# Kernel tuning notes

Measured on AMD Instinct MI355X. Metric: run time of the kernel, lower is better.

Reference implementation:

```python
import jax, jax.numpy as jnp
import numpy as np

B, T, E, H, D, NL = 2, 1024, 2048, 16, 128, 3
MAXL = T * (2 ** (NL - 1))  # k length doubles each layer: T, 2T, 4T


def _rms_norm(x, w, eps=1e-5):
    return x * jax.lax.rsqrt(jnp.mean(x * x, axis=-1, keepdims=True) + eps) * w


def _rope(x, cos, sin):
    # x: [B, S, H, D]; cos/sin: [>=S, D/2]; GPT-NeoX style (non-interleaved)
    S = x.shape[1]
    c = cos[:S][None, :, None, :]
    s = sin[:S][None, :, None, :]
    x1, x2 = jnp.split(x, 2, axis=-1)
    return jnp.concatenate([x1 * c - x2 * s, x1 * s + x2 * c], axis=-1)


def _causal_attn(q, k, v):
    # bottom-right-aligned causal (flash_attn_func causal=True with kv longer than q)
    Tq, L = q.shape[1], k.shape[1]
    scale = 1.0 / np.sqrt(q.shape[-1]).astype(np.float32)
    scores = jnp.einsum('bthd,bshd->bhts', q, k) * scale
    i = jnp.arange(Tq)[:, None]
    j = jnp.arange(L)[None, :]
    mask = j <= i + (L - Tq)
    scores = jnp.where(mask[None, None], scores, -jnp.inf)
    p = jax.nn.softmax(scores, axis=-1)
    return jnp.einsum('bhts,bshd->bthd', p, v)


def setup_inputs() -> dict:
    key = jax.random.key(0)
    ks = jax.random.split(key, 6)
    x = jax.random.normal(ks[0], (B, T, E), dtype=jnp.float32)
    inv_freq = 1.0 / (10000.0 ** (np.arange(0, D, 2, dtype=np.float32) / D))  # [D/2]
    ang = np.arange(MAXL, dtype=np.float32)[:, None] * inv_freq[None, :]      # [MAXL, D/2]
    cos = jnp.asarray(np.cos(ang), dtype=jnp.float32)
    sin = jnp.asarray(np.sin(ang), dtype=jnp.float32)
    wq = jax.random.normal(ks[1], (NL, E, E), dtype=jnp.float32) * 0.02
    wk = jax.random.normal(ks[2], (NL, E, E), dtype=jnp.float32) * 0.02
    wv = jax.random.normal(ks[3], (NL, E, E), dtype=jnp.float32) * 0.02
    ln_w = jnp.ones((NL, E), dtype=jnp.float32)
    lambdas = jnp.zeros((NL,), dtype=jnp.float32)
    w_out = jax.random.normal(ks[4], (E, E), dtype=jnp.float32) * 0.02
    final_ln_w = jnp.ones((E,), dtype=jnp.float32)
    alpha = jnp.ones((1,), dtype=jnp.float32)
    return {'x': x, 'cos': cos, 'sin': sin, 'wq': wq, 'wk': wk, 'wv': wv,
            'ln_w': ln_w, 'lambdas': lambdas, 'w_out': w_out,
            'final_ln_w': final_ln_w, 'alpha': alpha}


def reference(x, cos, sin, wq, wk, wv, ln_w, lambdas, w_out, final_ln_w, alpha):
    bsz, tgt_len, embed_dim = x.shape
    # lambda weights: sigmoid then LayerNorm over the NL scalars (no affine)
    lam = jax.nn.sigmoid(lambdas)
    lam = (lam - jnp.mean(lam)) * jax.lax.rsqrt(jnp.var(lam) + 1e-5)
    acc_k, acc_v = [], []
    total = jnp.zeros_like(x)
    for i in range(NL):  # small fixed layer count
        q = (x @ wq[i].T).reshape(bsz, tgt_len, H, D)
        k = (x @ wk[i].T).reshape(bsz, tgt_len, H, D)
        v = (x @ wv[i].T).reshape(bsz, tgt_len, H, D)
        if i > 0:
            k = jnp.concatenate([k] + acc_k, axis=1)
            v = jnp.concatenate([v] + acc_v, axis=1)
        q = _rope(q, cos, sin)
        k = _rope(k, cos, sin)  # note: cached K gets rotary re-applied, as in source
        attn = _causal_attn(q, k, v).reshape(bsz, tgt_len, embed_dim)
        attn = _rms_norm(attn, ln_w[i])
        total = total + attn * lam[i]
        acc_k.append(k)
        acc_v.append(v)
    out = _rms_norm(total + alpha * x, final_ln_w)
    return out @ w_out.T
```

## Files before the change

kernel.cpp:

```cpp
#include <hip/hip_runtime.h>

typedef unsigned short ushort_t;
typedef __attribute__((ext_vector_type(8))) short bf16x8;
typedef __attribute__((ext_vector_type(4))) short bf16x4;
typedef __attribute__((ext_vector_type(4))) float f32x4;
typedef __attribute__((ext_vector_type(4))) unsigned short u16x4;
typedef __attribute__((ext_vector_type(4))) unsigned int u32x4;

#define DEV __device__ __forceinline__

DEV ushort_t f2bf(float f) {
  union { float f; unsigned int u; } a; a.f = f;
  unsigned int u = a.u;
  unsigned int r = (u + 0x7fffu + ((u >> 16) & 1u)) >> 16;
  return (ushort_t)r;
}
DEV float bf2f(ushort_t b) {
  union { float f; unsigned int u; } a; a.u = ((unsigned int)b) << 16;
  return a.f;
}
DEV void gload_lds16(const void* g, void* l) {
  __builtin_amdgcn_global_load_lds((const __attribute__((address_space(1))) void*)g,
                                   (__attribute__((address_space(3))) void*)l, 16, 0, 0);
}
DEV bf16x4 tr16(const ushort_t* l) {
  unsigned a = (unsigned)(unsigned long long)(const __attribute__((address_space(3))) ushort_t*)l;
  bf16x4 d;
  asm volatile("ds_read_b64_tr_b16 %0, %1" : "=v"(d) : "v"(a));
  return d;
}
DEV bf16x8 ldsb128(const ushort_t* l) {
  unsigned a = (unsigned)(unsigned long long)(const __attribute__((address_space(3))) ushort_t*)l;
  bf16x8 d;
  asm volatile("ds_read_b128 %0, %1" : "=v"(d) : "v"(a));
  return d;
}

__global__ __launch_bounds__(256) void f2b_kernel(const float* __restrict__ in,
                                                  ushort_t* __restrict__ out, int n) {
  int base = (blockIdx.x * 256 + threadIdx.x) * 4;
  if (base >= n) return;
  f32x4 v = *(const f32x4*)(in + base);
  u16x4 o;
  o.x = f2bf(v.x); o.y = f2bf(v.y); o.z = f2bf(v.z); o.w = f2bf(v.w);
  *(u16x4*)(out + base) = o;
}

__global__ __launch_bounds__(256) void f2b3_kernel(const float* __restrict__ a, const float* __restrict__ b,
                                                   const float* __restrict__ c, ushort_t* __restrict__ out) {
  int id = blockIdx.x * 256 + threadIdx.x;
  int sel = id >> 20, k = (id & 1048575) * 4;
  const float* src = sel == 0 ? a : sel == 1 ? b : c;
  f32x4 v = *(const f32x4*)(src + k);
  u16x4 o;
  o.x = f2bf(v.x); o.y = f2bf(v.y); o.z = f2bf(v.z); o.w = f2bf(v.w);
  *(u16x4*)(out + (size_t)sel * 4194304 + k) = o;
}

__global__ void lam_kernel(const float* __restrict__ lambdas, float* __restrict__ lam) {
  if (threadIdx.x == 0 && blockIdx.x == 0) {
    float l0 = 1.f / (1.f + __expf(-lambdas[0]));
    float l1 = 1.f / (1.f + __expf(-lambdas[1]));
    float l2 = 1.f / (1.f + __expf(-lambdas[2]));
    float mean = (l0 + l1 + l2) * (1.f / 3.f);
    float d0 = l0 - mean, d1 = l1 - mean, d2 = l2 - mean;
    float var = (d0 * d0 + d1 * d1 + d2 * d2) * (1.f / 3.f);
    float rs = rsqrtf(var + 1e-5f);
    lam[0] = d0 * rs; lam[1] = d1 * rs; lam[2] = d2 * rs;
  }
}

DEV void gemm_core(const ushort_t* __restrict__ A, const ushort_t* __restrict__ Bm,
                   ushort_t* lsA, ushort_t* lsB, int bm, int bn, int kbeg, int kend,
                   f32x4 (&acc)[4][4]) {
  const int K = 2048;
  int tid = threadIdx.x;
  int w = tid >> 6, lane = tid & 63;
  int g = lane >> 4, r = lane & 15;
  int wm = w >> 1, wn = w & 1;
#pragma unroll
  for (int i = 0; i < 4; ++i)
#pragma unroll
    for (int j = 0; j < 4; ++j) acc[i][j] = 0.f;

  for (int kk = kbeg; kk < kend; kk += 32) {
    __syncthreads();
#pragma unroll
    for (int j2 = 0; j2 < 2; ++j2) {
      int eb = w * 1024 + j2 * 512;
      int ebl = eb + lane * 8;
      int rr = ebl >> 5, cc = ebl & 31;
      gload_lds16(A + (size_t)(bm * 128 + rr) * K + kk + cc, lsA + eb);
      gload_lds16(Bm + (size_t)(bn * 128 + rr) * K + kk + cc, lsB + eb);
    }
    __syncthreads();
    bf16x8 af[4], bfr[4];
#pragma unroll
    for (int i = 0; i < 4; ++i)
      af[i] = *(const bf16x8*)(lsA + (wm * 64 + i * 16 + r) * 32 + g * 8);
#pragma unroll
    for (int j = 0; j < 4; ++j)
      bfr[j] = *(const bf16x8*)(lsB + (wn * 64 + j * 16 + r) * 32 + g * 8);
#pragma unroll
    for (int i = 0; i < 4; ++i)
#pragma unroll
      for (int j = 0; j < 4; ++j)
        acc[i][j] = __builtin_amdgcn_mfma_f32_16x16x32_bf16(af[i], bfr[j], acc[i][j], 0, 0, 0);
  }
}

__global__ __launch_bounds__(256) void gemm_qkv(
    const ushort_t* __restrict__ A,
    const ushort_t* __restrict__ Bq, const ushort_t* __restrict__ Bk, const ushort_t* __restrict__ Bv,
    ushort_t* __restrict__ Cq, ushort_t* __restrict__ Ck, ushort_t* __restrict__ Cv, int Lkv) {
  __shared__ __align__(16) ushort_t lsA[4096];
  __shared__ __align__(16) ushort_t lsB[4096];
  int sel = blockIdx.x >> 4, bn = blockIdx.x & 15, bm = blockIdx.y;
  const ushort_t* Bm = (sel == 0) ? Bq : (sel == 1) ? Bk : Bv;
  ushort_t* C = (sel == 0) ? Cq : (sel == 1) ? Ck : Cv;
  int Lsel = (sel == 0) ? 1024 : Lkv;
  f32x4 acc[4][4];
  gemm_core(A, Bm, lsA, lsB, bm, bn, 0, 2048, acc);
  int lane = threadIdx.x & 63, w = threadIdx.x >> 6;
  int g = lane >> 4, r = lane & 15, wm = w >> 1, wn = w & 1;
#pragma unroll
  for (int i = 0; i < 4; ++i)
#pragma unroll
    for (int j = 0; j < 4; ++j) {
      int row0 = bm * 128 + wm * 64 + i * 16 + g * 4;
      int col = bn * 128 + wn * 64 + j * 16 + r;
#pragma unroll
      for (int t = 0; t < 4; ++t) {
        int row = row0 + t;
        int b2 = row >> 10, t2 = row & 1023;
        C[(size_t)(b2 * Lsel + t2) * 2048 + col] = f2bf(acc[i][j][t]);
      }
    }
}

__global__ __launch_bounds__(256) void gemm_bt_part(
    const ushort_t* __restrict__ A, const ushort_t* __restrict__ Bm, float* __restrict__ P) {
  __shared__ __align__(16) ushort_t lsA[4096];
  __shared__ __align__(16) ushort_t lsB[4096];
  int bn = blockIdx.x, bm = blockIdx.y, s = blockIdx.z;
  f32x4 acc[4][4];
  gemm_core(A, Bm, lsA, lsB, bm, bn, s * 1024, (s + 1) * 1024, acc);
  float* C = P + (size_t)s * 4194304;
  int lane = threadIdx.x & 63, w = threadIdx.x >> 6;
  int g = lane >> 4, r = lane & 15, wm = w >> 1, wn = w & 1;
#pragma unroll
  for (int i = 0; i < 4; ++i)
#pragma unroll
    for (int j = 0; j < 4; ++j) {
      int row0 = bm * 128 + wm * 64 + i * 16 + g * 4;
      int col = bn * 128 + wn * 64 + j * 16 + r;
#pragma unroll
      for (int t = 0; t < 4; ++t)
        C[(size_t)(row0 + t) * 2048 + col] = acc[i][j][t];
    }
}

__global__ __launch_bounds__(256) void add2_kernel(const float* __restrict__ a, const float* __restrict__ b,
                                                   float* __restrict__ out) {
  int i = (blockIdx.x * 256 + threadIdx.x) * 4;
  f32x4 va = *(const f32x4*)(a + i);
  f32x4 vb = *(const f32x4*)(b + i);
  f32x4 r;
#pragma unroll
  for (int k = 0; k < 4; ++k) r[k] = va[k] + vb[k];
  *(f32x4*)(out + i) = r;
}

DEV void rope_body(const ushort_t* src, ushort_t* dst, const float* cosT, const float* sinT,
                   int Ls, int s0, int Ld, int dpos0, int cnt, int bp) {
  int b = bp / cnt, pidx = bp % cnt;
  int pos = dpos0 + pidx;
  int pi = threadIdx.x * 4;
  int h = pi >> 6, d = pi & 63;
  const ushort_t* s_ = src + ((size_t)(b * Ls + s0 + pidx) * 16 + h) * 128 + d;
  ushort_t* d_ = dst + ((size_t)(b * Ld + pos) * 16 + h) * 128 + d;
  f32x4 c4 = *(const f32x4*)(cosT + (size_t)pos * 64 + d);
  f32x4 s4 = *(const f32x4*)(sinT + (size_t)pos * 64 + d);
  u16x4 x1 = *(const u16x4*)(s_);
  u16x4 x2 = *(const u16x4*)(s_ + 64);
  u16x4 o1, o2;
#pragma unroll
  for (int k = 0; k < 4; ++k) {
    float a = bf2f(x1[k]), bb = bf2f(x2[k]);
    o1[k] = f2bf(a * c4[k] - bb * s4[k]);
    o2[k] = f2bf(a * s4[k] + bb * c4[k]);
  }
  *(u16x4*)d_ = o1;
  *(u16x4*)(d_ + 64) = o2;
}
DEV void copy_body(const ushort_t* src, ushort_t* dst, int Ls, int s0, int Ld, int dpos0,
                   int cnt, int bp) {
  int b = bp / cnt, pidx = bp % cnt;
  const u32x4* s = (const u32x4*)(src + (size_t)(b * Ls + s0 + pidx) * 2048);
  u32x4* d = (u32x4*)(dst + (size_t)(b * Ld + dpos0 + pidx) * 2048);
  d[threadIdx.x] = s[threadIdx.x];
}

__global__ __launch_bounds__(256) void rope_qk(ushort_t* q, ushort_t* Kc,
                                               const float* __restrict__ cosT, const float* __restrict__ sinT,
                                               int L) {
  int bp = blockIdx.x;
  if (bp < 2048) rope_body(q, q, cosT, sinT, 1024, 0, 1024, 0, 1024, bp);
  else rope_body(Kc, Kc, cosT, sinT, L, 0, L, 0, 1024, bp - 2048);
}

__global__ __launch_bounds__(256) void layer1_cache(const ushort_t* __restrict__ K0, ushort_t* __restrict__ K1,
                                                    const ushort_t* __restrict__ V0, ushort_t* __restrict__ V1,
                                                    const float* __restrict__ cosT, const float* __restrict__ sinT) {
  int bp = blockIdx.x;
  if (bp < 2048) rope_body(K0, K1, cosT, sinT, 1024, 0, 2048, 1024, 1024, bp);
  else copy_body(V0, V1, 1024, 0, 2048, 1024, 1024, bp - 2048);
}

__global__ __launch_bounds__(256) void layer2_cache(const ushort_t* __restrict__ K1, ushort_t* __restrict__ K2,
                                                    const ushort_t* __restrict__ V1, ushort_t* __restrict__ V2,
                                                    const float* __restrict__ cosT, const float* __restrict__ sinT) {
  int bp = blockIdx.x;
  if (bp < 2048) copy_body(K1, K2, 2048, 1024, 4096, 1024, 1024, bp);
  else if (bp < 6144) rope_body(K1, K2, cosT, sinT, 2048, 0, 4096, 2048, 2048, bp - 2048);
  else if (bp < 8192) copy_body(V1, V2, 2048, 1024, 4096, 1024, 1024, bp - 6144);
  else copy_body(V1, V2, 2048, 0, 4096, 2048, 2048, bp - 8192);
}

__global__ __launch_bounds__(256, 4) void attn_kernel(
    const ushort_t* __restrict__ Q, const ushort_t* __restrict__ Kc, const ushort_t* __restrict__ Vc,
    ushort_t* __restrict__ Opart, float2* __restrict__ Ml, int Lk) {
  __shared__ __align__(16) ushort_t lsK[8192];
  __shared__ __align__(16) ushort_t lsV[8192];
  const float sc = 0.08838834764831843f;

  int bid = (int)blockIdx.x;
  int swz = (bid & 7) * 128 + (bid >> 3);
  int s = swz & 1;
  int rest = swz >> 1;

  int w = threadIdx.x >> 6, lane = threadIdx.x & 63;
  int bq = rest & 15, h = (rest >> 4) & 15, b = rest >> 8;
  int qt = bq * 4 + w;
  int g = lane >> 4, r = lane & 15;
  int off = Lk - 1024;

  const ushort_t* qbase = Q + ((size_t)(b * 1024 + qt * 16 + r) * 16 + h) * 128;
  bf16x8 qf[4];
#pragma unroll
  for (int c = 0; c < 4; ++c) qf[c] = *(const bf16x8*)(qbase + c * 32 + g * 8);

  int t = threadIdx.x;
  int krow0 = t >> 4,        kc0 = (t & 15) ^ (krow0 & 7);
  int krow1 = (t + 256) >> 4, kc1 = (t & 15) ^ (krow1 & 7);
  const size_t adv = 32 * 2048;
  const size_t adv2 = 2 * adv;
  const ushort_t* srcK0 = Kc + ((size_t)(b * Lk + krow0) * 16 + h) * 128 + kc0 * 8 + s * adv;
  const ushort_t* srcK1 = Kc + ((size_t)(b * Lk + krow1) * 16 + h) * 128 + kc1 * 8 + s * adv;
  int L0 = t, L1 = t + 256;
  int vrow0 = ((L0 >> 3) & 7) * 4 + ((L0 >> 1) & 3), vd0 = (L0 >> 6) * 16 + (L0 & 1) * 8;
  int vrow1 = ((L1 >> 3) & 7) * 4 + ((L1 >> 1) & 3), vd1 = (L1 >> 6) * 16 + (L1 & 1) * 8;
  const ushort_t* srcV0 = Vc + ((size_t)(b * Lk + vrow0) * 16 + h) * 128 + vd0 + s * adv;
  const ushort_t* srcV1 = Vc + ((size_t)(b * Lk + vrow1) * 16 + h) * 128 + vd1 + s * adv;

  auto STAGE = [&](int buf) {
    ushort_t* k0 = lsK + buf * 4096 + w * 512;
    ushort_t* v0 = lsV + buf * 4096 + w * 512;
    gload_lds16(srcK0, k0);
    gload_lds16(srcK1, k0 + 2048);
    gload_lds16(srcV0, v0);
    gload_lds16(srcV1, v0 + 2048);
    srcK0 += adv2; srcK1 += adv2; srcV0 += adv2; srcV1 += adv2;
  };

  float m_run = -1e30f, l_run = 0.f;
  f32x4 o[8];
#pragma unroll
  for (int c = 0; c < 8; ++c) o[c] = 0.f;

  int qp = qt * 16 + r + off;
  int nkt_w = ((qt * 16 + 15 + off) >> 5) + 1;
  int nkt_blk = (((bq * 4 + 3) * 16 + 15 + off) >> 5) + 1;
  int ntile = (nkt_blk - s + 1) >> 1;

  if (ntile > 0) {
    STAGE(0);
    for (int it = 0; it < ntile; ++it) {
      int kt = s + it * 2;
      int cur = it & 1;
      if (it + 1 < ntile) {
        STAGE(cur ^ 1);
        asm volatile("s_waitcnt vmcnt(4)" ::: "memory");
      } else {
        asm volatile("s_waitcnt vmcnt(0)" ::: "memory");
      }
      __builtin_amdgcn_s_barrier();
      __builtin_amdgcn_sched_barrier(0);
      if (kt < nkt_w) {
        const ushort_t* Kb = lsK + cur * 4096;
        const ushort_t* Vb = lsV + cur * 4096;
        f32x4 st[2];
#pragma unroll
        for (int ks = 0; ks < 2; ++ks) {
          bf16x8 kf[4];
#pragma unroll
          for (int c = 0; c < 4; ++c)
            kf[c] = ldsb128(Kb + (ks * 16 + r) * 128 + ((c * 32 + g * 8) ^ ((r & 7) * 8)));
          asm volatile("s_waitcnt lgkmcnt(0)" ::: "memory");
          __builtin_amdgcn_sched_barrier(0);
          __builtin_amdgcn_s_setprio(1);
          f32x4 acc = 0.f;
#pragma unroll
          for (int c = 0; c < 4; ++c)
            acc = __builtin_amdgcn_mfma_f32_16x16x32_bf16(kf[c], qf[c], acc, 0, 0, 0);
          __builtin_amdgcn_s_setprio(0);
          st[ks] = acc;
        }
        float pmax = -1e30f;
        int kp0 = kt * 32;
#pragma unroll
        for (int ks = 0; ks < 2; ++ks)
#pragma unroll
          for (int j = 0; j < 4; ++j) {
            int key = kp0 + ks * 16 + g * 4 + j;
            float sv = st[ks][j] * sc;
            if (key > qp) sv = -1e30f;
            st[ks][j] = sv;
            pmax = fmaxf(pmax, sv);
          }
        pmax = fmaxf(pmax, __shfl_xor(pmax, 16, 64));
        pmax = fmaxf(pmax, __shfl_xor(pmax, 32, 64));
        if (!__all(pmax <= m_run + 8.f)) {
          float mnew = fmaxf(m_run, pmax);
          float corr = __expf(m_run - mnew);
          l_run *= corr;
#pragma unroll
          for (int c = 0; c < 8; ++c)
#pragma unroll
            for (int tt = 0; tt < 4; ++tt) o[c][tt] *= corr;
          m_run = mnew;
        }
        float psum = 0.f;
        bf16x4 pf[2];
#pragma unroll
        for (int ks = 0; ks < 2; ++ks)
#pragma unroll
          for (int j = 0; j < 4; ++j) {
            float pe = __expf(st[ks][j] - m_run);
            psum += pe;
            pf[ks][j] = (short)f2bf(pe);
          }
        psum += __shfl_xor(psum, 16, 64);
        psum += __shfl_xor(psum, 32, 64);
        l_run += psum;
#pragma unroll
        for (int half = 0; half < 2; ++half) {
          bf16x4 vf[8];
#pragma unroll
          for (int i = 0; i < 8; ++i)
            vf[i] = tr16(Vb + (half * 4 + (i >> 1)) * 512 + (i & 1) * 256);
          asm volatile("s_waitcnt lgkmcnt(0)" ::: "memory");
          __builtin_amdgcn_sched_barrier(0);
          __builtin_amdgcn_s_setprio(1);
#pragma unroll
          for (int db = 0; db < 4; ++db) {
            int dblk = half * 4 + db;
            o[dblk] = __builtin_amdgcn_mfma_f32_16x16x16bf16_1k(vf[db * 2], pf[0], o[dblk], 0, 0, 0);
            o[dblk] = __builtin_amdgcn_mfma_f32_16x16x16bf16_1k(vf[db * 2 + 1], pf[1], o[dblk], 0, 0, 0);
          }
          __builtin_amdgcn_s_setprio(0);
        }
      }
      __builtin_amdgcn_sched_barrier(0);
      __builtin_amdgcn_s_barrier();
    }
  }
  ushort_t* ob = Opart + (size_t)s * 4194304 + ((size_t)(b * 1024 + qt * 16 + r) * 16 + h) * 128;
#pragma unroll
  for (int dblk = 0; dblk < 8; ++dblk) {
    u16x4 ov;
#pragma unroll
    for (int tt = 0; tt < 4; ++tt) ov[tt] = f2bf(o[dblk][tt]);
    *(u16x4*)(ob + dblk * 16 + g * 4) = ov;
  }
  if (g == 0) {
    float2 ml; ml.x = m_run; ml.y = l_run;
    Ml[((size_t)(s * 2 + b) * 1024 + qt * 16 + r) * 16 + h] = ml;
  }
}

template <int FIRST>
__global__ __launch_bounds__(256) void rms_combine(const ushort_t* __restrict__ Opart, const float2* __restrict__ Ml,
                                                   const float* __restrict__ lnw, const float* __restrict__ lam,
                                                   int li, float* __restrict__ total) {
  int row = blockIdx.x;
  int t8 = threadIdx.x * 8;
  int h = t8 >> 7;
  float2 ml0 = Ml[(size_t)row * 16 + h];
  float2 ml1 = Ml[(size_t)(row + 2048) * 16 + h];
  float M = fmaxf(ml0.x, ml1.x);
  float w0 = __expf(ml0.x - M), w1 = __expf(ml1.x - M);
  float rinv = 1.f / (w0 * ml0.y + w1 * ml1.y);
  w0 *= rinv; w1 *= rinv;
  const ushort_t* a0 = Opart + (size_t)row * 2048 + t8;
  const ushort_t* a1 = a0 + 4194304;
  u16x4 p00 = *(const u16x4*)(a0);
  u16x4 p01 = *(const u16x4*)(a0 + 4);
  u16x4 p10 = *(const u16x4*)(a1);
  u16x4 p11 = *(const u16x4*)(a1 + 4);
  f32x4 v0, v1;
#pragma unroll
  for (int k = 0; k < 4; ++k) {
    v0[k] = w0 * bf2f(p00[k]) + w1 * bf2f(p10[k]);
    v1[k] = w0 * bf2f(p01[k]) + w1 * bf2f(p11[k]);
  }
  float ss = v0.x * v0.x + v0.y * v0.y + v0.z * v0.z + v0.w * v0.w +
             v1.x * v1.x + v1.y * v1.y + v1.z * v1.z + v1.w * v1.w;
#pragma unroll
  for (int m = 1; m < 64; m <<= 1) ss += __shfl_xor(ss, m, 64);
  __shared__ float red[4];
  int w = threadIdx.x >> 6, lane = threadIdx.x & 63;
  if (lane == 0) red[w] = ss;
  __syncthreads();
  ss = red[0] + red[1] + red[2] + red[3];
  float sca = rsqrtf(ss * (1.f / 2048.f) + 1e-5f) * lam[li];
  f32x4 w0v = *(const f32x4*)(lnw + t8);
  f32x4 w1v = *(const f32x4*)(lnw + t8 + 4);
  float* o = total + (size_t)row * 2048 + t8;
  f32x4 r0, r1;
#pragma unroll
  for (int k = 0; k < 4; ++k) { r0[k] = v0[k] * sca * w0v[k]; r1[k] = v1[k] * sca * w1v[k]; }
  if (!FIRST) {
    f32x4 q0 = *(const f32x4*)(o);
    f32x4 q1 = *(const f32x4*)(o + 4);
#pragma unroll
    for (int k = 0; k < 4; ++k) { r0[k] += q0[k]; r1[k] += q1[k]; }
  }
  *(f32x4*)(o) = r0;
  *(f32x4*)(o + 4) = r1;
}

__global__ __launch_bounds__(256) void final_norm(const float* __restrict__ total, const float* __restrict__ x,
                                                  const float* __restrict__ alphap, const float* __restrict__ flw,
                                                  ushort_t* __restrict__ ybf) {
  int row = blockIdx.x;
  float al = alphap[0];
  int t8 = threadIdx.x * 8;
  const float* tp = total + (size_t)row * 2048 + t8;
  const float* xp = x + (size_t)row * 2048 + t8;
  f32x4 t0 = *(const f32x4*)(tp);
  f32x4 t1 = *(const f32x4*)(tp + 4);
  f32x4 x0 = *(const f32x4*)(xp);
  f32x4 x1 = *(const f32x4*)(xp + 4);
  float y[8];
#pragma unroll
  for (int k = 0; k < 4; ++k) { y[k] = t0[k] + al * x0[k]; y[4 + k] = t1[k] + al * x1[k]; }
  float ss = 0.f;
#pragma unroll
  for (int k = 0; k < 8; ++k) ss += y[k] * y[k];
#pragma unroll
  for (int m = 1; m < 64; m <<= 1) ss += __shfl_xor(ss, m, 64);
  __shared__ float red[4];
  int w = threadIdx.x >> 6, lane = threadIdx.x & 63;
  if (lane == 0) red[w] = ss;
  __syncthreads();
  ss = red[0] + red[1] + red[2] + red[3];
  float s = rsqrtf(ss * (1.f / 2048.f) + 1e-5f);
  f32x4 w0 = *(const f32x4*)(flw + t8);
  f32x4 w1 = *(const f32x4*)(flw + t8 + 4);
  u16x4 o0, o1;
#pragma unroll
  for (int k = 0; k < 4; ++k) {
    o0[k] = f2bf(y[k] * s * w0[k]);
    o1[k] = f2bf(y[4 + k] * s * w1[k]);
  }
  *(u16x4*)(ybf + (size_t)row * 2048 + t8) = o0;
  *(u16x4*)(ybf + (size_t)row * 2048 + t8 + 4) = o1;
}

extern "C" void kernel_launch(void* const* d_in, const int* in_sizes, int n_in,
                              void* d_out, int out_size, void* d_ws, size_t ws_size,
                              hipStream_t stream) {
  const float* x = (const float*)d_in[0];
  const float* cosT = (const float*)d_in[1];
  const float* sinT = (const float*)d_in[2];
  const float* wq = (const float*)d_in[3];
  const float* wk = (const float*)d_in[4];
  const float* wv = (const float*)d_in[5];
  const float* lnw = (const float*)d_in[6];
  const float* lambdas = (const float*)d_in[7];
  const float* w_out = (const float*)d_in[8];
  const float* flw = (const float*)d_in[9];
  const float* alpha = (const float*)d_in[10];

  const size_t ME = 4194304ull;
  char* p = (char*)d_ws;
  size_t off = 0;
  auto alc = [&](size_t bytes) -> void* {
    void* r = p + off;
    off += (bytes + 255) & ~(size_t)255;
    return r;
  };
  ushort_t* xb = (ushort_t*)alc(ME * 2);
  void* uni = alc(2 * ME * 4);
  ushort_t* wl = (ushort_t*)uni;
  ushort_t* Opart = (ushort_t*)uni;
  float* Ppart = (float*)uni;
  ushort_t* q = (ushort_t*)alc(ME * 2);
  ushort_t* K0 = (ushort_t*)alc(ME * 2);
  ushort_t* K1 = (ushort_t*)alc(2 * ME * 2);
  ushort_t* K2 = (ushort_t*)alc(4 * ME * 2);
  ushort_t* V0 = (ushort_t*)alc(ME * 2);
  ushort_t* V1 = (ushort_t*)alc(2 * ME * 2);
  ushort_t* V2 = (ushort_t*)alc(4 * ME * 2);
  float* total = (float*)alc(ME * 4);
  float2* Ml = (float2*)alc(65536 * 8);
  float* lam = (float*)alc(256);
  ushort_t* ybf = q;
  ushort_t* wob = K0;

  f2b_kernel<<<4096, 256, 0, stream>>>(x, xb, 4194304);
  lam_kernel<<<1, 64, 0, stream>>>(lambdas, lam);

  ushort_t* Kc[3] = {K0, K1, K2};
  ushort_t* Vc[3] = {V0, V1, V2};

  for (int li = 0; li < 3; ++li) {
    int L = 1024 << li;
    size_t woff = (size_t)li * ME;
    f2b3_kernel<<<12288, 256, 0, stream>>>(wq + woff, wk + woff, wv + woff, wl);
    gemm_qkv<<<dim3(48, 16), 256, 0, stream>>>(xb, wl, wl + ME, wl + 2 * ME,
                                               q, Kc[li], Vc[li], L);
    rope_qk<<<4096, 256, 0, stream>>>(q, Kc[li], cosT, sinT, L);
    if (li == 1)
      layer1_cache<<<4096, 256, 0, stream>>>(K0, K1, V0, V1, cosT, sinT);
    else if (li == 2)
      layer2_cache<<<12288, 256, 0, stream>>>(K1, K2, V1, V2, cosT, sinT);
    attn_kernel<<<1024, 256, 0, stream>>>(q, Kc[li], Vc[li], Opart, Ml, L);
    if (li == 0)
      rms_combine<1><<<2048, 256, 0, stream>>>(Opart, Ml, lnw, lam, 0, total);
    else
      rms_combine<0><<<2048, 256, 0, stream>>>(Opart, Ml, lnw + (size_t)li * 2048, lam, li, total);
  }

  f2b_kernel<<<4096, 256, 0, stream>>>(w_out, wob, 4194304);
  final_norm<<<2048, 256, 0, stream>>>(total, x, alpha, flw, ybf);
  gemm_bt_part<<<dim3(16, 16, 2), 256, 0, stream>>>(ybf, wob, Ppart);
  add2_kernel<<<4096, 256, 0, stream>>>(Ppart, Ppart + ME, (float*)d_out);
}
```

Before: 580.3 us.

## Fuse Q rotary and softmax scale into attention, use exp2 and immediate LDS offsets

Applies rotary embedding to Q while it is loaded in the attention kernel, folding the softmax scale and log2(e) into the cos/sin factors. The separate rope pass then only processes K. Softmax switches to exp2 (and the combine kernel follows), the causal mask is skipped for tiles that are fully visible, and LDS reads use precomputed bases with immediate offsets to cut address arithmetic. The costs are extra cos/sin global loads per attention block and an extra rounding of Q to bf16 after the scale is folded in.

```diff
diff --git a/kernel.cpp b/kernel.cpp
--- a/kernel.cpp
+++ b/kernel.cpp
@@ -1,4 +1,5 @@
 #include <hip/hip_runtime.h>
+#include <hip/hip_bf16.h>
 
 typedef unsigned short ushort_t;
 typedef __attribute__((ext_vector_type(8))) short bf16x8;
@@ -10,10 +11,8 @@
 #define DEV __device__ __forceinline__
 
 DEV ushort_t f2bf(float f) {
-  union { float f; unsigned int u; } a; a.f = f;
-  unsigned int u = a.u;
-  unsigned int r = (u + 0x7fffu + ((u >> 16) & 1u)) >> 16;
-  return (ushort_t)r;
+  __hip_bfloat16 h = __float2bfloat16(f);
+  return __builtin_bit_cast(unsigned short, h);
 }
 DEV float bf2f(ushort_t b) {
   union { float f; unsigned int u; } a; a.u = ((unsigned int)b) << 16;
@@ -23,16 +22,19 @@
   __builtin_amdgcn_global_load_lds((const __attribute__((address_space(1))) void*)g,
                                    (__attribute__((address_space(3))) void*)l, 16, 0, 0);
 }
-DEV bf16x4 tr16(const ushort_t* l) {
-  unsigned a = (unsigned)(unsigned long long)(const __attribute__((address_space(3))) ushort_t*)l;
+DEV unsigned ldsaddr(const void* l) {
+  return (unsigned)(unsigned long long)(const __attribute__((address_space(3))) void*)l;
+}
+template <int OFF>
+DEV bf16x4 tr16o(unsigned a) {
   bf16x4 d;
-  asm volatile("ds_read_b64_tr_b16 %0, %1" : "=v"(d) : "v"(a));
+  asm volatile("ds_read_b64_tr_b16 %0, %1 offset:%c2" : "=v"(d) : "v"(a), "i"(OFF));
   return d;
 }
-DEV bf16x8 ldsb128(const ushort_t* l) {
-  unsigned a = (unsigned)(unsigned long long)(const __attribute__((address_space(3))) ushort_t*)l;
+template <int OFF>
+DEV bf16x8 ldsb128o(unsigned a) {
   bf16x8 d;
-  asm volatile("ds_read_b128 %0, %1" : "=v"(d) : "v"(a));
+  asm volatile("ds_read_b128 %0, %1 offset:%c2" : "=v"(d) : "v"(a), "i"(OFF));
   return d;
 }
 
@@ -201,12 +203,9 @@
   d[threadIdx.x] = s[threadIdx.x];
 }
 
-__global__ __launch_bounds__(256) void rope_qk(ushort_t* q, ushort_t* Kc,
-                                               const float* __restrict__ cosT, const float* __restrict__ sinT,
-                                               int L) {
-  int bp = blockIdx.x;
-  if (bp < 2048) rope_body(q, q, cosT, sinT, 1024, 0, 1024, 0, 1024, bp);
-  else rope_body(Kc, Kc, cosT, sinT, L, 0, L, 0, 1024, bp - 2048);
+__global__ __launch_bounds__(256) void rope_k(ushort_t* Kc, const float* __restrict__ cosT,
+                                              const float* __restrict__ sinT, int L) {
+  rope_body(Kc, Kc, cosT, sinT, L, 0, L, 0, 1024, blockIdx.x);
 }
 
 __global__ __launch_bounds__(256) void layer1_cache(const ushort_t* __restrict__ K0, ushort_t* __restrict__ K1,
@@ -228,11 +227,12 @@
 }
 
 __global__ __launch_bounds__(256, 4) void attn_kernel(
-    const ushort_t* __restrict__ Q, const ushort_t* __restrict__ Kc, const ushort_t* __restrict__ Vc,
+    const ushort_t* __restrict__ Qraw, const ushort_t* __restrict__ Kc, const ushort_t* __restrict__ Vc,
+    const float* __restrict__ cosT, const float* __restrict__ sinT,
     ushort_t* __restrict__ Opart, float2* __restrict__ Ml, int Lk) {
   __shared__ __align__(16) ushort_t lsK[8192];
   __shared__ __align__(16) ushort_t lsV[8192];
-  const float sc = 0.08838834764831843f;
+  const float SC2 = 0.1275174366f;
 
   int bid = (int)blockIdx.x;
   int swz = (bid & 7) * 128 + (bid >> 3);
@@ -245,10 +245,32 @@
   int g = lane >> 4, r = lane & 15;
   int off = Lk - 1024;
 
-  const ushort_t* qbase = Q + ((size_t)(b * 1024 + qt * 16 + r) * 16 + h) * 128;
+  const ushort_t* qbase = Qraw + ((size_t)(b * 1024 + qt * 16 + r) * 16 + h) * 128;
+  int pos = qt * 16 + r;
+  const float* cb = cosT + (size_t)pos * 64;
+  const float* sb = sinT + (size_t)pos * 64;
   bf16x8 qf[4];
 #pragma unroll
-  for (int c = 0; c < 4; ++c) qf[c] = *(const bf16x8*)(qbase + c * 32 + g * 8);
+  for (int c = 0; c < 2; ++c) {
+    int d0 = c * 32 + g * 8;
+    f32x4 c0 = *(const f32x4*)(cb + d0);
+    f32x4 c1 = *(const f32x4*)(cb + d0 + 4);
+    f32x4 s0 = *(const f32x4*)(sb + d0);
+    f32x4 s1 = *(const f32x4*)(sb + d0 + 4);
+    bf16x8 x1 = *(const bf16x8*)(qbase + d0);
+    bf16x8 x2 = *(const bf16x8*)(qbase + d0 + 64);
+    bf16x8 lo, hi;
+#pragma unroll
+    for (int k = 0; k < 8; ++k) {
+      float cv = (k < 4 ? c0[k] : c1[k - 4]) * SC2;
+      float sv = (k < 4 ? s0[k] : s1[k - 4]) * SC2;
+      float a = bf2f((ushort_t)x1[k]);
+      float bb = bf2f((ushort_t)x2[k]);
+      lo[k] = (short)f2bf(a * cv - bb * sv);
+      hi[k] = (short)f2bf(a * sv + bb * cv);
+    }
+    qf[c] = lo; qf[c + 2] = hi;
+  }
 
   int t = threadIdx.x;
   int krow0 = t >> 4,        kc0 = (t & 15) ^ (krow0 & 7);
@@ -273,15 +295,26 @@
     srcK0 += adv2; srcK1 += adv2; srcV0 += adv2; srcV1 += adv2;
   };
 
+  unsigned kx[4];
+  unsigned kbase0 = ldsaddr(lsK) + (unsigned)(r * 256);
+#pragma unroll
+  for (int c = 0; c < 4; ++c)
+    kx[c] = kbase0 + (unsigned)((((c * 32 + g * 8) ^ ((r & 7) * 8))) * 2);
+  unsigned vbase0 = ldsaddr(lsV);
+
   float m_run = -1e30f, l_run = 0.f;
   f32x4 o[8];
 #pragma unroll
   for (int c = 0; c < 8; ++c) o[c] = 0.f;
 
   int qp = qt * 16 + r + off;
+  int qmin = qt * 16 + off;
   int nkt_w = ((qt * 16 + 15 + off) >> 5) + 1;
   int nkt_blk = (((bq * 4 + 3) * 16 + 15 + off) >> 5) + 1;
   int ntile = (nkt_blk - s + 1) >> 1;
+
+#define LDK(c, ks) ldsb128o<(ks) * 4096>(kx[c] + kb)
+#define LDV(hh, i) tr16o<(hh) * 4096 + (i) * 512>(vb)
 
   if (ntile > 0) {
     STAGE(0);
@@ -297,42 +330,59 @@
       __builtin_amdgcn_s_barrier();
       __builtin_amdgcn_sched_barrier(0);
       if (kt < nkt_w) {
-        const ushort_t* Kb = lsK + cur * 4096;
-        const ushort_t* Vb = lsV + cur * 4096;
+        unsigned kb = (unsigned)(cur << 13);
+        unsigned vb = vbase0 + kb;
         f32x4 st[2];
-#pragma unroll
-        for (int ks = 0; ks < 2; ++ks) {
-          bf16x8 kf[4];
-#pragma unroll
-          for (int c = 0; c < 4; ++c)
-            kf[c] = ldsb128(Kb + (ks * 16 + r) * 128 + ((c * 32 + g * 8) ^ ((r & 7) * 8)));
+        {
+          bf16x8 k0 = LDK(0, 0), k1 = LDK(1, 0), k2 = LDK(2, 0), k3 = LDK(3, 0);
           asm volatile("s_waitcnt lgkmcnt(0)" ::: "memory");
           __builtin_amdgcn_sched_barrier(0);
           __builtin_amdgcn_s_setprio(1);
           f32x4 acc = 0.f;
-#pragma unroll
-          for (int c = 0; c < 4; ++c)
-            acc = __builtin_amdgcn_mfma_f32_16x16x32_bf16(kf[c], qf[c], acc, 0, 0, 0);
+          acc = __builtin_amdgcn_mfma_f32_16x16x32_bf16(k0, qf[0], acc, 0, 0, 0);
+          acc = __builtin_amdgcn_mfma_f32_16x16x32_bf16(k1, qf[1], acc, 0, 0, 0);
+          acc = __builtin_amdgcn_mfma_f32_16x16x32_bf16(k2, qf[2], acc, 0, 0, 0);
+          acc = __builtin_amdgcn_mfma_f32_16x16x32_bf16(k3, qf[3], acc, 0, 0, 0);
           __builtin_amdgcn_s_setprio(0);
-          st[ks] = acc;
+          st[0] = acc;
+        }
+        {
+          bf16x8 k0 = LDK(0, 1), k1 = LDK(1, 1), k2 = LDK(2, 1), k3 = LDK(3, 1);
+          asm volatile("s_waitcnt lgkmcnt(0)" ::: "memory");
+          __builtin_amdgcn_sched_barrier(0);
+          __builtin_amdgcn_s_setprio(1);
+          f32x4 acc = 0.f;
+          acc = __builtin_amdgcn_mfma_f32_16x16x32_bf16(k0, qf[0], acc, 0, 0, 0);
+          acc = __builtin_amdgcn_mfma_f32_16x16x32_bf16(k1, qf[1], acc, 0, 0, 0);
+          acc = __builtin_amdgcn_mfma_f32_16x16x32_bf16(k2, qf[2], acc, 0, 0, 0);
+          acc = __builtin_amdgcn_mfma_f32_16x16x32_bf16(k3, qf[3], acc, 0, 0, 0);
+          __builtin_amdgcn_s_setprio(0);
+          st[1] = acc;
         }
         float pmax = -1e30f;
         int kp0 = kt * 32;
-#pragma unroll
-        for (int ks = 0; ks < 2; ++ks)
-#pragma unroll
-          for (int j = 0; j < 4; ++j) {
-            int key = kp0 + ks * 16 + g * 4 + j;
-            float sv = st[ks][j] * sc;
-            if (key > qp) sv = -1e30f;
-            st[ks][j] = sv;
-            pmax = fmaxf(pmax, sv);
-          }
+        if (kp0 + 31 > qmin) {
+#pragma unroll
+          for (int ks = 0; ks < 2; ++ks)
+#pragma unroll
+            for (int j = 0; j < 4; ++j) {
+              int key = kp0 + ks * 16 + g * 4 + j;
+              float sv = st[ks][j];
+              if (key > qp) sv = -1e30f;
+              st[ks][j] = sv;
+              pmax = fmaxf(pmax, sv);
+            }
+        } else {
+#pragma unroll
+          for (int ks = 0; ks < 2; ++ks)
+#pragma unroll
+            for (int j = 0; j < 4; ++j) pmax = fmaxf(pmax, st[ks][j]);
+        }
         pmax = fmaxf(pmax, __shfl_xor(pmax, 16, 64));
         pmax = fmaxf(pmax, __shfl_xor(pmax, 32, 64));
-        if (!__all(pmax <= m_run + 8.f)) {
+        if (!__all(pmax <= m_run + 11.5f)) {
           float mnew = fmaxf(m_run, pmax);
-          float corr = __expf(m_run - mnew);
+          float corr = exp2f(m_run - mnew);
           l_run *= corr;
 #pragma unroll
           for (int c = 0; c < 8; ++c)
@@ -346,28 +396,43 @@
         for (int ks = 0; ks < 2; ++ks)
 #pragma unroll
           for (int j = 0; j < 4; ++j) {
-            float pe = __expf(st[ks][j] - m_run);
+            float pe = exp2f(st[ks][j] - m_run);
             psum += pe;
             pf[ks][j] = (short)f2bf(pe);
           }
         psum += __shfl_xor(psum, 16, 64);
         psum += __shfl_xor(psum, 32, 64);
         l_run += psum;
-#pragma unroll
-        for (int half = 0; half < 2; ++half) {
-          bf16x4 vf[8];
-#pragma unroll
-          for (int i = 0; i < 8; ++i)
-            vf[i] = tr16(Vb + (half * 4 + (i >> 1)) * 512 + (i & 1) * 256);
+        {
+          bf16x4 v0 = LDV(0, 0), v1 = LDV(0, 1), v2 = LDV(0, 2), v3 = LDV(0, 3);
+          bf16x4 v4 = LDV(0, 4), v5 = LDV(0, 5), v6 = LDV(0, 6), v7 = LDV(0, 7);
           asm volatile("s_waitcnt lgkmcnt(0)" ::: "memory");
           __builtin_amdgcn_sched_barrier(0);
           __builtin_amdgcn_s_setprio(1);
-#pragma unroll
-          for (int db = 0; db < 4; ++db) {
-            int dblk = half * 4 + db;
-            o[dblk] = __builtin_amdgcn_mfma_f32_16x16x16bf16_1k(vf[db * 2], pf[0], o[dblk], 0, 0, 0);
-            o[dblk] = __builtin_amdgcn_mfma_f32_16x16x16bf16_1k(vf[db * 2 + 1], pf[1], o[dblk], 0, 0, 0);
-          }
+          o[0] = __builtin_amdgcn_mfma_f32_16x16x16bf16_1k(v0, pf[0], o[0], 0, 0, 0);
+          o[0] = __builtin_amdgcn_mfma_f32_16x16x16bf16_1k(v1, pf[1], o[0], 0, 0, 0);
+          o[1] = __builtin_amdgcn_mfma_f32_16x16x16bf16_1k(v2, pf[0], o[1], 0, 0, 0);
+          o[1] = __builtin_amdgcn_mfma_f32_16x16x16bf16_1k(v3, pf[1], o[1], 0, 0, 0);
+          o[2] = __builtin_amdgcn_mfma_f32_16x16x16bf16_1k(v4, pf[0], o[2], 0, 0, 0);
+          o[2] = __builtin_amdgcn_mfma_f32_16x16x16bf16_1k(v5, pf[1], o[2], 0, 0, 0);
+          o[3] = __builtin_amdgcn_mfma_f32_16x16x16bf16_1k(v6, pf[0], o[3], 0, 0, 0);
+          o[3] = __builtin_amdgcn_mfma_f32_16x16x16bf16_1k(v7, pf[1], o[3], 0, 0, 0);
+          __builtin_amdgcn_s_setprio(0);
+        }
+        {
+          bf16x4 v0 = LDV(1, 0), v1 = LDV(1, 1), v2 = LDV(1, 2), v3 = LDV(1, 3);
+          bf16x4 v4 = LDV(1, 4), v5 = LDV(1, 5), v6 = LDV(1, 6), v7 = LDV(1, 7);
+          asm volatile("s_waitcnt lgkmcnt(0)" ::: "memory");
+          __builtin_amdgcn_sched_barrier(0);
+          __builtin_amdgcn_s_setprio(1);
+          o[4] = __builtin_amdgcn_mfma_f32_16x16x16bf16_1k(v0, pf[0], o[4], 0, 0, 0);
+          o[4] = __builtin_amdgcn_mfma_f32_16x16x16bf16_1k(v1, pf[1], o[4], 0, 0, 0);
+          o[5] = __builtin_amdgcn_mfma_f32_16x16x16bf16_1k(v2, pf[0], o[5], 0, 0, 0);
+          o[5] = __builtin_amdgcn_mfma_f32_16x16x16bf16_1k(v3, pf[1], o[5], 0, 0, 0);
+          o[6] = __builtin_amdgcn_mfma_f32_16x16x16bf16_1k(v4, pf[0], o[6], 0, 0, 0);
+          o[6] = __builtin_amdgcn_mfma_f32_16x16x16bf16_1k(v5, pf[1], o[6], 0, 0, 0);
+          o[7] = __builtin_amdgcn_mfma_f32_16x16x16bf16_1k(v6, pf[0], o[7], 0, 0, 0);
+          o[7] = __builtin_amdgcn_mfma_f32_16x16x16bf16_1k(v7, pf[1], o[7], 0, 0, 0);
           __builtin_amdgcn_s_setprio(0);
         }
       }
@@ -375,6 +440,8 @@
       __builtin_amdgcn_s_barrier();
     }
   }
+#undef LDK
+#undef LDV
   ushort_t* ob = Opart + (size_t)s * 4194304 + ((size_t)(b * 1024 + qt * 16 + r) * 16 + h) * 128;
 #pragma unroll
   for (int dblk = 0; dblk < 8; ++dblk) {
@@ -399,7 +466,7 @@
   float2 ml0 = Ml[(size_t)row * 16 + h];
   float2 ml1 = Ml[(size_t)(row + 2048) * 16 + h];
   float M = fmaxf(ml0.x, ml1.x);
-  float w0 = __expf(ml0.x - M), w1 = __expf(ml1.x - M);
+  float w0 = exp2f(ml0.x - M), w1 = exp2f(ml1.x - M);
   float rinv = 1.f / (w0 * ml0.y + w1 * ml1.y);
   w0 *= rinv; w1 *= rinv;
   const ushort_t* a0 = Opart + (size_t)row * 2048 + t8;
@@ -531,12 +598,12 @@
     f2b3_kernel<<<12288, 256, 0, stream>>>(wq + woff, wk + woff, wv + woff, wl);
     gemm_qkv<<<dim3(48, 16), 256, 0, stream>>>(xb, wl, wl + ME, wl + 2 * ME,
                                                q, Kc[li], Vc[li], L);
-    rope_qk<<<4096, 256, 0, stream>>>(q, Kc[li], cosT, sinT, L);
+    rope_k<<<2048, 256, 0, stream>>>(Kc[li], cosT, sinT, L);
     if (li == 1)
       layer1_cache<<<4096, 256, 0, stream>>>(K0, K1, V0, V1, cosT, sinT);
     else if (li == 2)
       layer2_cache<<<12288, 256, 0, stream>>>(K1, K2, V1, V2, cosT, sinT);
-    attn_kernel<<<1024, 256, 0, stream>>>(q, Kc[li], Vc[li], Opart, Ml, L);
+    attn_kernel<<<1024, 256, 0, stream>>>(q, Kc[li], Vc[li], cosT, sinT, Opart, Ml, L);
     if (li == 0)
       rms_combine<1><<<2048, 256, 0, stream>>>(Opart, Ml, lnw, lam, 0, total);
     else
```

Measured after the change: 560.8 us. -3.4%, faster.
